# Kernel tuning notes

Hardware: AMD Instinct MI355X
Metric: run time of the kernel (lower is better)

The kernel has to match this reference:

```python
import jax, jax.numpy as jnp
import numpy as np
import math

B, S, HID, NH = 2, 2048, 1024, 16
HD = HID // NH  # head_dim = 64
TEMPERATURE = 1.0


def setup_inputs() -> dict:
    key = jax.random.key(0)
    ks = jax.random.split(key, 6)
    w = lambda k: (jax.random.normal(k, (HID, HID), dtype=jnp.float32) * 0.02)
    return {
        "hidden_states": jax.random.normal(ks[0], (B, S, HID), dtype=jnp.float32),
        "attention_mask": jnp.ones((B, S), dtype=jnp.float32),
        "Wq": w(ks[1]), "bq": jnp.zeros((HID,), jnp.float32),
        "Wk": w(ks[2]), "bk": jnp.zeros((HID,), jnp.float32),
        "Wv": w(ks[3]), "bv": jnp.zeros((HID,), jnp.float32),
        "Wo": w(ks[4]), "bo": jnp.zeros((HID,), jnp.float32),
    }


def reference(hidden_states, attention_mask, Wq, bq, Wk, bk, Wv, bv, Wo, bo):
    b, s, hid = hidden_states.shape
    heads = lambda x: x.reshape(b, s, NH, HD).transpose(0, 2, 1, 3)  # [b,h,s,d]

    q = heads(hidden_states @ Wq.T + bq)
    k = heads(hidden_states @ Wk.T + bk)
    v = heads(hidden_states @ Wv.T + bv)

    # padding mask applied multiplicatively to k and v
    m = attention_mask[:, None, :, None]  # [b,1,s,1]
    k = k * m
    v = v * m

    # auxiliary Hopfield state: k^T @ v per head -> [b,h,d,d]
    state = jnp.einsum("bhsd,bhse->bhde", k, v)

    # energy / scores
    energy = jnp.einsum("bhqd,bhkd->bhqk", q, k) / (TEMPERATURE * math.sqrt(HD))
    causal = jnp.triu(jnp.ones((s, s), dtype=bool), k=1)  # True above diagonal
    energy = jnp.where(causal[None, None], -jnp.inf, energy)
    energy = jnp.where(attention_mask[:, None, None, :] == 0, -jnp.inf, energy)

    attn = jax.nn.softmax(energy, axis=-1)
    out = jnp.einsum("bhqk,bhkd->bhqd", attn, v)
    out = out.transpose(0, 2, 1, 3).reshape(b, s, hid)
    out = out @ Wo.T + bo
    return out, state
```

## Files before the change

### kernel.cpp

```cpp
#include <hip/hip_runtime.h>
#include <hip/hip_bf16.h>

#define B_ 2
#define S_ 2048
#define HID_ 1024
#define NH_ 16
#define HD_ 64
#define MTOK (B_*S_)
#define LDQKV 3072

typedef __attribute__((ext_vector_type(8))) __bf16 bf16x8;
typedef __attribute__((ext_vector_type(4))) __bf16 bf16x4;
typedef __attribute__((ext_vector_type(4))) float f32x4;

__device__ __forceinline__ void gl16(__bf16* lds, const __bf16* g) {
  __builtin_amdgcn_global_load_lds(
      (const __attribute__((address_space(1))) void*)g,
      (__attribute__((address_space(3))) void*)lds, 16, 0, 0);
}
__device__ __forceinline__ void gl4(float* lds, const float* g) {
  __builtin_amdgcn_global_load_lds(
      (const __attribute__((address_space(1))) void*)g,
      (__attribute__((address_space(3))) void*)lds, 4, 0, 0);
}

__global__ __launch_bounds__(256) void cast_all(
    const float* __restrict__ X,
    const float* __restrict__ Wq, const float* __restrict__ Wk,
    const float* __restrict__ Wv, const float* __restrict__ Wo,
    __bf16* __restrict__ Xb, __bf16* __restrict__ Wqkvb, __bf16* __restrict__ Wob)
{
  int i = blockIdx.x * 256 + threadIdx.x;
  const float* src; __bf16* dst; int j;
  if (i < (1 << 20))              { src = X;  dst = Xb;                 j = i; }
  else if (i < (1<<20)+(1<<18))   { src = Wq; dst = Wqkvb;              j = i - (1<<20); }
  else if (i < (1<<20)+(2<<18))   { src = Wk; dst = Wqkvb + (1<<20);    j = i - (1<<20) - (1<<18); }
  else if (i < (1<<20)+(3<<18))   { src = Wv; dst = Wqkvb + (2<<20);    j = i - (1<<20) - (2<<18); }
  else                            { src = Wo; dst = Wob;                j = i - (1<<20) - (3<<18); }
  float4 v = reinterpret_cast<const float4*>(src)[j];
  bf16x4 o;
  o[0] = (__bf16)v.x; o[1] = (__bf16)v.y; o[2] = (__bf16)v.z; o[3] = (__bf16)v.w;
  reinterpret_cast<bf16x4*>(dst)[j] = o;
}

__global__ __launch_bounds__(256) void gemm_qkv(
    const __bf16* __restrict__ A, const __bf16* __restrict__ W,
    const float* __restrict__ bq, const float* __restrict__ bk,
    const float* __restrict__ bv, const float* __restrict__ mask,
    __bf16* __restrict__ C)
{
  __shared__ __bf16 As[128 * 32];
  __shared__ __bf16 Bs[128 * 32];
  const int t = threadIdx.x;
  const int m0 = blockIdx.y * 128;
  const int n0 = blockIdx.x * 128;
  const int lane = t & 63;
  const int w = t >> 6;
  const int wr = (w >> 1) * 64;
  const int wc = (w & 1) * 64;
  const int fr = lane & 15;
  const int kg = lane >> 4;

  f32x4 acc[4][4];
  #pragma unroll
  for (int i = 0; i < 4; i++)
    #pragma unroll
    for (int j = 0; j < 4; j++) acc[i][j] = (f32x4)0.f;

  const int srow = w * 16 + (lane >> 2);
  const int scol = (lane & 3) * 8;
  const __bf16* ap0 = A + (size_t)(m0 + srow) * HID_ + scol;
  const __bf16* ap1 = A + (size_t)(m0 + 64 + srow) * HID_ + scol;
  const __bf16* wp0 = W + (size_t)(n0 + srow) * HID_ + scol;
  const __bf16* wp1 = W + (size_t)(n0 + 64 + srow) * HID_ + scol;

  for (int k0 = 0; k0 < HID_; k0 += 32) {
    __syncthreads();
    gl16(&As[w * 512], ap0 + k0);
    gl16(&As[2048 + w * 512], ap1 + k0);
    gl16(&Bs[w * 512], wp0 + k0);
    gl16(&Bs[2048 + w * 512], wp1 + k0);
    __syncthreads();
    bf16x8 af[4], bf[4];
    #pragma unroll
    for (int m = 0; m < 4; m++) af[m] = *(const bf16x8*)&As[(wr + m*16 + fr) * 32 + kg*8];
    #pragma unroll
    for (int n = 0; n < 4; n++) bf[n] = *(const bf16x8*)&Bs[(wc + n*16 + fr) * 32 + kg*8];
    #pragma unroll
    for (int m = 0; m < 4; m++)
      #pragma unroll
      for (int n = 0; n < 4; n++)
        acc[m][n] = __builtin_amdgcn_mfma_f32_16x16x32_bf16(af[m], bf[n], acc[m][n], 0, 0, 0);
  }

  const int region = n0 >> 10;
  const float* bias = region == 0 ? bq : (region == 1 ? bk : bv);
  const int nloc = n0 & 1023;

  #pragma unroll
  for (int m = 0; m < 4; m++) {
    #pragma unroll
    for (int r = 0; r < 4; r++) {
      int row = m0 + wr + m*16 + kg*4 + r;
      float rs = region ? mask[row] : 1.f;
      #pragma unroll
      for (int n = 0; n < 4; n++) {
        int c = wc + n*16 + fr;
        float v = (acc[m][n][r] + bias[nloc + c]) * rs;
        C[(size_t)row * LDQKV + n0 + c] = (__bf16)v;
      }
    }
  }
}

__global__ __launch_bounds__(256) void gemm_o(
    const __bf16* __restrict__ A, const __bf16* __restrict__ W,
    const float* __restrict__ bias, float* __restrict__ C)
{
  __shared__ __bf16 As[128 * 32];
  __shared__ __bf16 Bs[128 * 32];
  const int t = threadIdx.x;
  const int m0 = blockIdx.y * 128;
  const int n0 = blockIdx.x * 128;
  const int lane = t & 63;
  const int w = t >> 6;
  const int wr = (w >> 1) * 64;
  const int wc = (w & 1) * 64;
  const int fr = lane & 15;
  const int kg = lane >> 4;

  f32x4 acc[4][4];
  #pragma unroll
  for (int i = 0; i < 4; i++)
    #pragma unroll
    for (int j = 0; j < 4; j++) acc[i][j] = (f32x4)0.f;

  const int srow = w * 16 + (lane >> 2);
  const int scol = (lane & 3) * 8;
  const __bf16* ap0 = A + (size_t)(m0 + srow) * HID_ + scol;
  const __bf16* ap1 = A + (size_t)(m0 + 64 + srow) * HID_ + scol;
  const __bf16* wp0 = W + (size_t)(n0 + srow) * HID_ + scol;
  const __bf16* wp1 = W + (size_t)(n0 + 64 + srow) * HID_ + scol;

  for (int k0 = 0; k0 < HID_; k0 += 32) {
    __syncthreads();
    gl16(&As[w * 512], ap0 + k0);
    gl16(&As[2048 + w * 512], ap1 + k0);
    gl16(&Bs[w * 512], wp0 + k0);
    gl16(&Bs[2048 + w * 512], wp1 + k0);
    __syncthreads();
    bf16x8 af[4], bf[4];
    #pragma unroll
    for (int m = 0; m < 4; m++) af[m] = *(const bf16x8*)&As[(wr + m*16 + fr) * 32 + kg*8];
    #pragma unroll
    for (int n = 0; n < 4; n++) bf[n] = *(const bf16x8*)&Bs[(wc + n*16 + fr) * 32 + kg*8];
    #pragma unroll
    for (int m = 0; m < 4; m++)
      #pragma unroll
      for (int n = 0; n < 4; n++)
        acc[m][n] = __builtin_amdgcn_mfma_f32_16x16x32_bf16(af[m], bf[n], acc[m][n], 0, 0, 0);
  }

  #pragma unroll
  for (int m = 0; m < 4; m++) {
    #pragma unroll
    for (int r = 0; r < 4; r++) {
      int row = m0 + wr + m*16 + kg*4 + r;
      #pragma unroll
      for (int n = 0; n < 4; n++) {
        int col = n0 + wc + n*16 + fr;
        C[(size_t)row * HID_ + col] = acc[m][n][r] + bias[col];
      }
    }
  }
}

__global__ __launch_bounds__(256) void transpose_bf16(
    const __bf16* __restrict__ in, int ldin, __bf16* __restrict__ out)
{
  __shared__ __bf16 tile[64][68];
  const int tok0 = blockIdx.x * 64;
  const int f0 = blockIdx.y * 64;
  const int t = threadIdx.x;
  const int r = t >> 2;
  const int c0 = (t & 3) * 16;
  const __bf16* src = in + (size_t)(tok0 + r) * ldin + f0 + c0;
  *(bf16x8*)&tile[r][c0]     = *(const bf16x8*)src;
  *(bf16x8*)&tile[r][c0 + 8] = *(const bf16x8*)(src + 8);
  __syncthreads();
  bf16x8 o0, o1;
  #pragma unroll
  for (int j = 0; j < 8; j++) { o0[j] = tile[c0 + j][r]; o1[j] = tile[c0 + 8 + j][r]; }
  __bf16* dst = out + (size_t)(f0 + r) * MTOK + tok0 + c0;
  *(bf16x8*)dst = o0;
  *(bf16x8*)(dst + 8) = o1;
}

#define SCALE_LOG2E 0.18033688011112043f

__device__ __forceinline__ bf16x8 ld_swz(const __bf16* base, int row, int xb) {
  return *(const bf16x8*)((const char*)base + row * 128 + (xb ^ ((row & 7) << 4)));
}
__device__ __forceinline__ void st_swz16(__bf16* base, int row, int colbyte, __bf16 v) {
  *(__bf16*)((char*)base + row * 128 + (colbyte ^ ((row & 7) << 4))) = v;
}
__device__ __forceinline__ bf16x8 ld_swz256(const __bf16* base, int row, int xb) {
  return *(const bf16x8*)((const char*)base + row * 256 + (xb ^ ((row & 7) << 4)));
}

__global__ __launch_bounds__(512) void flash_mfma(
    const __bf16* __restrict__ Q, const __bf16* __restrict__ K,
    const __bf16* __restrict__ Vt, const float* __restrict__ mask,
    __bf16* __restrict__ O)
{
  __shared__ __bf16 Ks[2][64 * 64];
  __shared__ __bf16 Vs[2][64 * 64];
  __shared__ __bf16 Ps[8][16 * 64];
  __shared__ float mk[2][64];

  const int bh = blockIdx.x;
  const int qt = (int)(gridDim.y - 1) - (int)blockIdx.y;
  const int b = bh >> 4, h = bh & 15;
  const int t = threadIdx.x;
  const int w = t >> 6;
  const int lane = t & 63;
  const int fc = lane & 15;
  const int kg = lane >> 4;
  const int g4 = kg * 4;

  const int q0w = qt * 128 + w * 16;
  const size_t tokbase = (size_t)b * S_;

  const int rr = lane >> 3;
  const int cswz = ((lane & 7) ^ rr) * 8;
  const int ktmax = 2 * qt + 1;

  gl16(&Ks[0][w * 512], K + (tokbase + (size_t)(w * 8 + rr)) * LDQKV + h * HD_ + cswz);
  gl16(&Vs[0][w * 512], Vt + (size_t)(h * HD_ + w * 8 + rr) * MTOK + tokbase + cswz);
  gl4(&mk[0][0], mask + tokbase + lane);

  bf16x8 qa[2];
  {
    const __bf16* qp = Q + (tokbase + q0w + fc) * LDQKV + h * HD_;
    qa[0] = *(const bf16x8*)(qp + kg * 8);
    qa[1] = *(const bf16x8*)(qp + 32 + kg * 8);
  }

  bf16x8 ones;
  #pragma unroll
  for (int j = 0; j < 8; j++) ones[j] = (__bf16)1.f;

  f32x4 acc[4], accl;
  #pragma unroll
  for (int n = 0; n < 4; n++) acc[n] = (f32x4)0.f;
  accl = (f32x4)0.f;

  __bf16* pw = &Ps[w][0];

  for (int kt = 0; kt <= ktmax; ++kt) {
    const int cur = kt & 1;
    if (kt < ktmax) {
      const int nxt = cur ^ 1;
      gl16(&Ks[nxt][w * 512],
           K + (tokbase + (size_t)((kt + 1) * 64 + w * 8 + rr)) * LDQKV + h * HD_ + cswz);
      gl16(&Vs[nxt][w * 512],
           Vt + (size_t)(h * HD_ + w * 8 + rr) * MTOK + tokbase + (kt + 1) * 64 + cswz);
      gl4(&mk[nxt][0], mask + tokbase + (kt + 1) * 64 + lane);
      asm volatile("s_waitcnt vmcnt(3)" ::: "memory");
    } else {
      asm volatile("s_waitcnt vmcnt(0)" ::: "memory");
    }
    __builtin_amdgcn_sched_barrier(0);
    __builtin_amdgcn_s_barrier();

    if (kt * 64 <= q0w + 15) {
      const __bf16* ks = &Ks[cur][0];
      const __bf16* vs = &Vs[cur][0];
      f32x4 s[4];
      #pragma unroll
      for (int n = 0; n < 4; n++) s[n] = (f32x4)0.f;
      #pragma unroll
      for (int kd = 0; kd < 2; kd++)
        #pragma unroll
        for (int n = 0; n < 4; n++) {
          bf16x8 kf = ld_swz(ks, n * 16 + fc, kd * 64 + kg * 16);
          s[n] = __builtin_amdgcn_mfma_f32_16x16x32_bf16(qa[kd], kf, s[n], 0, 0, 0);
        }

      bool okm[4];
      #pragma unroll
      for (int n = 0; n < 4; n++) okm[n] = (mk[cur][n * 16 + fc] != 0.f);

      const bool fullt = (kt * 64 + 63 <= q0w);
      if (fullt) {
        #pragma unroll
        for (int r = 0; r < 4; r++)
          #pragma unroll
          for (int n = 0; n < 4; n++) {
            float p = okm[n] ? exp2f(s[n][r] * SCALE_LOG2E) : 0.f;
            st_swz16(pw, g4 + r, (n * 16 + fc) * 2, (__bf16)p);
          }
      } else {
        #pragma unroll
        for (int r = 0; r < 4; r++) {
          const int qg = q0w + g4 + r;
          #pragma unroll
          for (int n = 0; n < 4; n++) {
            bool ok = okm[n] && (kt * 64 + n * 16 + fc <= qg);
            float p = ok ? exp2f(s[n][r] * SCALE_LOG2E) : 0.f;
            st_swz16(pw, g4 + r, (n * 16 + fc) * 2, (__bf16)p);
          }
        }
      }

      #pragma unroll
      for (int kc = 0; kc < 2; kc++) {
        bf16x8 pf = ld_swz(pw, fc, kc * 64 + kg * 16);
        accl = __builtin_amdgcn_mfma_f32_16x16x32_bf16(pf, ones, accl, 0, 0, 0);
        #pragma unroll
        for (int n = 0; n < 4; n++) {
          bf16x8 vf = ld_swz(vs, n * 16 + fc, kc * 64 + kg * 16);
          acc[n] = __builtin_amdgcn_mfma_f32_16x16x32_bf16(pf, vf, acc[n], 0, 0, 0);
        }
      }
    }
    __builtin_amdgcn_s_barrier();
  }

  #pragma unroll
  for (int r = 0; r < 4; r++) {
    float inv = accl[r] > 0.f ? 1.f / accl[r] : 0.f;
    __bf16* op = O + (tokbase + q0w + g4 + r) * HID_ + h * HD_;
    #pragma unroll
    for (int n = 0; n < 4; n++)
      op[n * 16 + fc] = (__bf16)(acc[n][r] * inv);
  }
}

__global__ __launch_bounds__(256) void state_mfma(
    const __bf16* __restrict__ Kt, const __bf16* __restrict__ Vt,
    float* __restrict__ part)
{
  __shared__ __bf16 Kl[64 * 128];
  __shared__ __bf16 Vl[64 * 128];
  const int bh = blockIdx.x, sc = blockIdx.y;
  const int b = bh >> 4, h = bh & 15;
  const int t = threadIdx.x;
  const int w = t >> 6;
  const int lane = t & 63;
  const int fc = lane & 15;
  const int kg = lane >> 4;
  const size_t colbase = (size_t)b * S_ + sc * 128;
  const int rloc = lane >> 4;
  const int cb = (lane & 15) * 16;

  #pragma unroll
  for (int c = 0; c < 4; c++) {
    int row = w * 16 + c * 4 + rloc;
    int scol = (cb ^ ((row & 7) << 4)) >> 1;
    gl16(&Kl[(w * 16 + c * 4) * 128], Kt + (size_t)(h * HD_ + row) * MTOK + colbase + scol);
    gl16(&Vl[(w * 16 + c * 4) * 128], Vt + (size_t)(h * HD_ + row) * MTOK + colbase + scol);
  }
  __syncthreads();

  f32x4 acc[4];
  #pragma unroll
  for (int n = 0; n < 4; n++) acc[n] = (f32x4)0.f;
  #pragma unroll
  for (int ks = 0; ks < 4; ks++) {
    bf16x8 af = ld_swz256(Kl, w * 16 + fc, ks * 64 + kg * 16);
    #pragma unroll
    for (int n = 0; n < 4; n++) {
      bf16x8 bfr = ld_swz256(Vl, n * 16 + fc, ks * 64 + kg * 16);
      acc[n] = __builtin_amdgcn_mfma_f32_16x16x32_bf16(af, bfr, acc[n], 0, 0, 0);
    }
  }

  float* dst = part + (((size_t)bh * 16 + sc) << 12);
  #pragma unroll
  for (int n = 0; n < 4; n++)
    #pragma unroll
    for (int r = 0; r < 4; r++)
      dst[(w * 16 + kg * 4 + r) * 64 + n * 16 + fc] = acc[n][r];
}

__global__ __launch_bounds__(256) void state_reduce(
    const float* __restrict__ part, float* __restrict__ out)
{
  int i = blockIdx.x * 256 + threadIdx.x;
  int bh = i >> 12, de = i & 4095;
  float s = 0.f;
  #pragma unroll
  for (int sc = 0; sc < 16; sc++) s += part[(((size_t)bh * 16 + sc) << 12) + de];
  out[i] = s;
}

extern "C" void kernel_launch(void* const* d_in, const int* in_sizes, int n_in,
                              void* d_out, int out_size, void* d_ws, size_t ws_size,
                              hipStream_t stream)
{
  const float* hs   = (const float*)d_in[0];
  const float* mask = (const float*)d_in[1];
  const float* Wq   = (const float*)d_in[2];
  const float* bq   = (const float*)d_in[3];
  const float* Wk   = (const float*)d_in[4];
  const float* bk   = (const float*)d_in[5];
  const float* Wv   = (const float*)d_in[6];
  const float* bv   = (const float*)d_in[7];
  const float* Wo   = (const float*)d_in[8];
  const float* bo   = (const float*)d_in[9];
  float* out = (float*)d_out;

  char* ws = (char*)d_ws;
  __bf16* Wqkvb = (__bf16*)(ws);
  __bf16* Wob   = (__bf16*)(ws + (6u  << 20));
  __bf16* Xb    = (__bf16*)(ws + (8u  << 20));
  __bf16* QKV   = (__bf16*)(ws + (16u << 20));
  __bf16* Ob    = (__bf16*)(ws + (40u << 20));
  float*  part  = (float*)(ws + (48u << 20));

  cast_all<<<8192, 256, 0, stream>>>(hs, Wq, Wk, Wv, Wo, Xb, Wqkvb, Wob);

  gemm_qkv<<<dim3(LDQKV / 128, MTOK / 128), 256, 0, stream>>>(
      Xb, Wqkvb, bq, bk, bv, mask, QKV);

  __bf16* Vtg = Xb;
  transpose_bf16<<<dim3(MTOK / 64, HID_ / 64), 256, 0, stream>>>(QKV + 2048, LDQKV, Vtg);

  flash_mfma<<<dim3(B_ * NH_, S_ / 128), 512, 0, stream>>>(
      QKV, QKV + 1024, Vtg, mask, Ob);

  gemm_o<<<dim3(HID_ / 128, MTOK / 128), 256, 0, stream>>>(Ob, Wob, bo, out);

  __bf16* Ktg = Wqkvb;
  transpose_bf16<<<dim3(MTOK / 64, HID_ / 64), 256, 0, stream>>>(QKV + 1024, LDQKV, Ktg);

  state_mfma<<<dim3(B_ * NH_, 16), 256, 0, stream>>>(Ktg, Vtg, part);
  state_reduce<<<512, 256, 0, stream>>>(part, out + (size_t)MTOK * HID_);
}
```

Before: 144.1 us.

## Double-buffer GEMM loads, shrink flash tiles to 64 queries, merge K/V transposes

```diff
diff --git a/kernel.cpp b/kernel.cpp
--- a/kernel.cpp
+++ b/kernel.cpp
@@ -49,8 +49,8 @@
     const float* __restrict__ bv, const float* __restrict__ mask,
     __bf16* __restrict__ C)
 {
-  __shared__ __bf16 As[128 * 32];
-  __shared__ __bf16 Bs[128 * 32];
+  __shared__ __bf16 As[2][128 * 32];
+  __shared__ __bf16 Bs[2][128 * 32];
   const int t = threadIdx.x;
   const int m0 = blockIdx.y * 128;
   const int n0 = blockIdx.x * 128;
@@ -74,23 +74,34 @@
   const __bf16* wp0 = W + (size_t)(n0 + srow) * HID_ + scol;
   const __bf16* wp1 = W + (size_t)(n0 + 64 + srow) * HID_ + scol;
 
+  #define GSTAGE(buf, koff) \
+    gl16(&As[buf][w * 512], ap0 + (koff)); \
+    gl16(&As[buf][2048 + w * 512], ap1 + (koff)); \
+    gl16(&Bs[buf][w * 512], wp0 + (koff)); \
+    gl16(&Bs[buf][2048 + w * 512], wp1 + (koff));
+
+  GSTAGE(0, 0);
   for (int k0 = 0; k0 < HID_; k0 += 32) {
-    __syncthreads();
-    gl16(&As[w * 512], ap0 + k0);
-    gl16(&As[2048 + w * 512], ap1 + k0);
-    gl16(&Bs[w * 512], wp0 + k0);
-    gl16(&Bs[2048 + w * 512], wp1 + k0);
-    __syncthreads();
+    const int cur = (k0 >> 5) & 1;
+    if (k0 + 32 < HID_) {
+      GSTAGE(cur ^ 1, k0 + 32);
+      asm volatile("s_waitcnt vmcnt(4)" ::: "memory");
+    } else {
+      asm volatile("s_waitcnt vmcnt(0)" ::: "memory");
+    }
+    __builtin_amdgcn_sched_barrier(0);
+    __builtin_amdgcn_s_barrier();
     bf16x8 af[4], bf[4];
     #pragma unroll
-    for (int m = 0; m < 4; m++) af[m] = *(const bf16x8*)&As[(wr + m*16 + fr) * 32 + kg*8];
-    #pragma unroll
-    for (int n = 0; n < 4; n++) bf[n] = *(const bf16x8*)&Bs[(wc + n*16 + fr) * 32 + kg*8];
+    for (int m = 0; m < 4; m++) af[m] = *(const bf16x8*)&As[cur][(wr + m*16 + fr) * 32 + kg*8];
+    #pragma unroll
+    for (int n = 0; n < 4; n++) bf[n] = *(const bf16x8*)&Bs[cur][(wc + n*16 + fr) * 32 + kg*8];
     #pragma unroll
     for (int m = 0; m < 4; m++)
       #pragma unroll
       for (int n = 0; n < 4; n++)
         acc[m][n] = __builtin_amdgcn_mfma_f32_16x16x32_bf16(af[m], bf[n], acc[m][n], 0, 0, 0);
+    __builtin_amdgcn_s_barrier();
   }
 
   const int region = n0 >> 10;
@@ -117,8 +128,8 @@
     const __bf16* __restrict__ A, const __bf16* __restrict__ W,
     const float* __restrict__ bias, float* __restrict__ C)
 {
-  __shared__ __bf16 As[128 * 32];
-  __shared__ __bf16 Bs[128 * 32];
+  __shared__ __bf16 As[2][128 * 32];
+  __shared__ __bf16 Bs[2][128 * 32];
   const int t = threadIdx.x;
   const int m0 = blockIdx.y * 128;
   const int n0 = blockIdx.x * 128;
@@ -142,23 +153,28 @@
   const __bf16* wp0 = W + (size_t)(n0 + srow) * HID_ + scol;
   const __bf16* wp1 = W + (size_t)(n0 + 64 + srow) * HID_ + scol;
 
+  GSTAGE(0, 0);
   for (int k0 = 0; k0 < HID_; k0 += 32) {
-    __syncthreads();
-    gl16(&As[w * 512], ap0 + k0);
-    gl16(&As[2048 + w * 512], ap1 + k0);
-    gl16(&Bs[w * 512], wp0 + k0);
-    gl16(&Bs[2048 + w * 512], wp1 + k0);
-    __syncthreads();
+    const int cur = (k0 >> 5) & 1;
+    if (k0 + 32 < HID_) {
+      GSTAGE(cur ^ 1, k0 + 32);
+      asm volatile("s_waitcnt vmcnt(4)" ::: "memory");
+    } else {
+      asm volatile("s_waitcnt vmcnt(0)" ::: "memory");
+    }
+    __builtin_amdgcn_sched_barrier(0);
+    __builtin_amdgcn_s_barrier();
     bf16x8 af[4], bf[4];
     #pragma unroll
-    for (int m = 0; m < 4; m++) af[m] = *(const bf16x8*)&As[(wr + m*16 + fr) * 32 + kg*8];
-    #pragma unroll
-    for (int n = 0; n < 4; n++) bf[n] = *(const bf16x8*)&Bs[(wc + n*16 + fr) * 32 + kg*8];
+    for (int m = 0; m < 4; m++) af[m] = *(const bf16x8*)&As[cur][(wr + m*16 + fr) * 32 + kg*8];
+    #pragma unroll
+    for (int n = 0; n < 4; n++) bf[n] = *(const bf16x8*)&Bs[cur][(wc + n*16 + fr) * 32 + kg*8];
     #pragma unroll
     for (int m = 0; m < 4; m++)
       #pragma unroll
       for (int n = 0; n < 4; n++)
         acc[m][n] = __builtin_amdgcn_mfma_f32_16x16x32_bf16(af[m], bf[n], acc[m][n], 0, 0, 0);
+    __builtin_amdgcn_s_barrier();
   }
 
   #pragma unroll
@@ -175,16 +191,19 @@
   }
 }
 
-__global__ __launch_bounds__(256) void transpose_bf16(
-    const __bf16* __restrict__ in, int ldin, __bf16* __restrict__ out)
+__global__ __launch_bounds__(256) void transpose_kv(
+    const __bf16* __restrict__ Kin, const __bf16* __restrict__ Vin,
+    __bf16* __restrict__ Kt, __bf16* __restrict__ Vt)
 {
   __shared__ __bf16 tile[64][68];
   const int tok0 = blockIdx.x * 64;
   const int f0 = blockIdx.y * 64;
+  const __bf16* in = blockIdx.z ? Vin : Kin;
+  __bf16* out = blockIdx.z ? Vt : Kt;
   const int t = threadIdx.x;
   const int r = t >> 2;
   const int c0 = (t & 3) * 16;
-  const __bf16* src = in + (size_t)(tok0 + r) * ldin + f0 + c0;
+  const __bf16* src = in + (size_t)(tok0 + r) * LDQKV + f0 + c0;
   *(bf16x8*)&tile[r][c0]     = *(const bf16x8*)src;
   *(bf16x8*)&tile[r][c0 + 8] = *(const bf16x8*)(src + 8);
   __syncthreads();
@@ -208,18 +227,70 @@
   return *(const bf16x8*)((const char*)base + row * 256 + (xb ^ ((row & 7) << 4)));
 }
 
-__global__ __launch_bounds__(512) void flash_mfma(
+__device__ __forceinline__ void attn_tile(
+    const __bf16* __restrict__ ks, const __bf16* __restrict__ vs,
+    const bool (&okm)[4], __bf16* __restrict__ pw,
+    const bf16x8 (&qa)[2], f32x4 (&acc)[4], f32x4& accl,
+    const bf16x8 ones, int q0w, int kt, int fc, int kg)
+{
+  f32x4 s[4];
+  #pragma unroll
+  for (int n = 0; n < 4; n++) s[n] = (f32x4)0.f;
+  #pragma unroll
+  for (int kd = 0; kd < 2; kd++)
+    #pragma unroll
+    for (int n = 0; n < 4; n++) {
+      bf16x8 kf = ld_swz(ks, n * 16 + fc, kd * 64 + kg * 16);
+      s[n] = __builtin_amdgcn_mfma_f32_16x16x32_bf16(qa[kd], kf, s[n], 0, 0, 0);
+    }
+
+  const int g4 = kg * 4;
+  const bool fullt = (kt * 64 + 63 <= q0w);
+  if (fullt) {
+    #pragma unroll
+    for (int r = 0; r < 4; r++)
+      #pragma unroll
+      for (int n = 0; n < 4; n++) {
+        float p = okm[n] ? exp2f(s[n][r] * SCALE_LOG2E) : 0.f;
+        st_swz16(pw, g4 + r, (n * 16 + fc) * 2, (__bf16)p);
+      }
+  } else {
+    #pragma unroll
+    for (int r = 0; r < 4; r++) {
+      const int qg = q0w + g4 + r;
+      #pragma unroll
+      for (int n = 0; n < 4; n++) {
+        bool ok = okm[n] && (kt * 64 + n * 16 + fc <= qg);
+        float p = ok ? exp2f(s[n][r] * SCALE_LOG2E) : 0.f;
+        st_swz16(pw, g4 + r, (n * 16 + fc) * 2, (__bf16)p);
+      }
+    }
+  }
+
+  #pragma unroll
+  for (int kc = 0; kc < 2; kc++) {
+    bf16x8 pf = ld_swz(pw, fc, kc * 64 + kg * 16);
+    accl = __builtin_amdgcn_mfma_f32_16x16x32_bf16(pf, ones, accl, 0, 0, 0);
+    #pragma unroll
+    for (int n = 0; n < 4; n++) {
+      bf16x8 vf = ld_swz(vs, n * 16 + fc, kc * 64 + kg * 16);
+      acc[n] = __builtin_amdgcn_mfma_f32_16x16x32_bf16(pf, vf, acc[n], 0, 0, 0);
+    }
+  }
+}
+
+__global__ __launch_bounds__(256) void flash_mfma(
     const __bf16* __restrict__ Q, const __bf16* __restrict__ K,
     const __bf16* __restrict__ Vt, const float* __restrict__ mask,
     __bf16* __restrict__ O)
 {
   __shared__ __bf16 Ks[2][64 * 64];
   __shared__ __bf16 Vs[2][64 * 64];
-  __shared__ __bf16 Ps[8][16 * 64];
+  __shared__ __bf16 Ps[4][16 * 64];
   __shared__ float mk[2][64];
 
   const int bh = blockIdx.x;
-  const int qt = (int)(gridDim.y - 1) - (int)blockIdx.y;
+  const int qt = 31 - (int)blockIdx.y;
   const int b = bh >> 4, h = bh & 15;
   const int t = threadIdx.x;
   const int w = t >> 6;
@@ -228,15 +299,17 @@
   const int kg = lane >> 4;
   const int g4 = kg * 4;
 
-  const int q0w = qt * 128 + w * 16;
+  const int q0w = qt * 64 + w * 16;
   const size_t tokbase = (size_t)b * S_;
 
   const int rr = lane >> 3;
   const int cswz = ((lane & 7) ^ rr) * 8;
-  const int ktmax = 2 * qt + 1;
-
-  gl16(&Ks[0][w * 512], K + (tokbase + (size_t)(w * 8 + rr)) * LDQKV + h * HD_ + cswz);
-  gl16(&Vs[0][w * 512], Vt + (size_t)(h * HD_ + w * 8 + rr) * MTOK + tokbase + cswz);
+  const int ktmax = qt;
+
+  gl16(&Ks[0][(w * 16) * 64],     K + (tokbase + (size_t)(w * 16 + rr)) * LDQKV + h * HD_ + cswz);
+  gl16(&Ks[0][(w * 16 + 8) * 64], K + (tokbase + (size_t)(w * 16 + 8 + rr)) * LDQKV + h * HD_ + cswz);
+  gl16(&Vs[0][(w * 16) * 64],     Vt + (size_t)(h * HD_ + w * 16 + rr) * MTOK + tokbase + cswz);
+  gl16(&Vs[0][(w * 16 + 8) * 64], Vt + (size_t)(h * HD_ + w * 16 + 8 + rr) * MTOK + tokbase + cswz);
   gl4(&mk[0][0], mask + tokbase + lane);
 
   bf16x8 qa[2];
@@ -261,69 +334,25 @@
     const int cur = kt & 1;
     if (kt < ktmax) {
       const int nxt = cur ^ 1;
-      gl16(&Ks[nxt][w * 512],
-           K + (tokbase + (size_t)((kt + 1) * 64 + w * 8 + rr)) * LDQKV + h * HD_ + cswz);
-      gl16(&Vs[nxt][w * 512],
-           Vt + (size_t)(h * HD_ + w * 8 + rr) * MTOK + tokbase + (kt + 1) * 64 + cswz);
+      const size_t krow = tokbase + (size_t)((kt + 1) * 64);
+      gl16(&Ks[nxt][(w * 16) * 64],     K + (krow + w * 16 + rr) * LDQKV + h * HD_ + cswz);
+      gl16(&Ks[nxt][(w * 16 + 8) * 64], K + (krow + w * 16 + 8 + rr) * LDQKV + h * HD_ + cswz);
+      gl16(&Vs[nxt][(w * 16) * 64],     Vt + (size_t)(h * HD_ + w * 16 + rr) * MTOK + tokbase + (kt + 1) * 64 + cswz);
+      gl16(&Vs[nxt][(w * 16 + 8) * 64], Vt + (size_t)(h * HD_ + w * 16 + 8 + rr) * MTOK + tokbase + (kt + 1) * 64 + cswz);
       gl4(&mk[nxt][0], mask + tokbase + (kt + 1) * 64 + lane);
-      asm volatile("s_waitcnt vmcnt(3)" ::: "memory");
+      asm volatile("s_waitcnt vmcnt(5)" ::: "memory");
     } else {
       asm volatile("s_waitcnt vmcnt(0)" ::: "memory");
     }
     __builtin_amdgcn_sched_barrier(0);
     __builtin_amdgcn_s_barrier();
 
-    if (kt * 64 <= q0w + 15) {
-      const __bf16* ks = &Ks[cur][0];
-      const __bf16* vs = &Vs[cur][0];
-      f32x4 s[4];
-      #pragma unroll
-      for (int n = 0; n < 4; n++) s[n] = (f32x4)0.f;
-      #pragma unroll
-      for (int kd = 0; kd < 2; kd++)
-        #pragma unroll
-        for (int n = 0; n < 4; n++) {
-          bf16x8 kf = ld_swz(ks, n * 16 + fc, kd * 64 + kg * 16);
-          s[n] = __builtin_amdgcn_mfma_f32_16x16x32_bf16(qa[kd], kf, s[n], 0, 0, 0);
-        }
-
-      bool okm[4];
-      #pragma unroll
-      for (int n = 0; n < 4; n++) okm[n] = (mk[cur][n * 16 + fc] != 0.f);
-
-      const bool fullt = (kt * 64 + 63 <= q0w);
-      if (fullt) {
-        #pragma unroll
-        for (int r = 0; r < 4; r++)
-          #pragma unroll
-          for (int n = 0; n < 4; n++) {
-            float p = okm[n] ? exp2f(s[n][r] * SCALE_LOG2E) : 0.f;
-            st_swz16(pw, g4 + r, (n * 16 + fc) * 2, (__bf16)p);
-          }
-      } else {
-        #pragma unroll
-        for (int r = 0; r < 4; r++) {
-          const int qg = q0w + g4 + r;
-          #pragma unroll
-          for (int n = 0; n < 4; n++) {
-            bool ok = okm[n] && (kt * 64 + n * 16 + fc <= qg);
-            float p = ok ? exp2f(s[n][r] * SCALE_LOG2E) : 0.f;
-            st_swz16(pw, g4 + r, (n * 16 + fc) * 2, (__bf16)p);
-          }
-        }
-      }
-
-      #pragma unroll
-      for (int kc = 0; kc < 2; kc++) {
-        bf16x8 pf = ld_swz(pw, fc, kc * 64 + kg * 16);
-        accl = __builtin_amdgcn_mfma_f32_16x16x32_bf16(pf, ones, accl, 0, 0, 0);
-        #pragma unroll
-        for (int n = 0; n < 4; n++) {
-          bf16x8 vf = ld_swz(vs, n * 16 + fc, kc * 64 + kg * 16);
-          acc[n] = __builtin_amdgcn_mfma_f32_16x16x32_bf16(pf, vf, acc[n], 0, 0, 0);
-        }
-      }
-    }
+    bool okm[4];
+    #pragma unroll
+    for (int n = 0; n < 4; n++) okm[n] = (mk[cur][n * 16 + fc] != 0.f);
+
+    attn_tile(&Ks[cur][0], &Vs[cur][0], okm, pw, qa, acc, accl, ones, q0w, kt, fc, kg);
+
     __builtin_amdgcn_s_barrier();
   }
 
@@ -417,7 +446,7 @@
   __bf16* Xb    = (__bf16*)(ws + (8u  << 20));
   __bf16* QKV   = (__bf16*)(ws + (16u << 20));
   __bf16* Ob    = (__bf16*)(ws + (40u << 20));
-  float*  part  = (float*)(ws + (48u << 20));
+  __bf16* Ktg   = (__bf16*)(ws + (48u << 20));
 
   cast_all<<<8192, 256, 0, stream>>>(hs, Wq, Wk, Wv, Wo, Xb, Wqkvb, Wob);
 
@@ -425,16 +454,15 @@
       Xb, Wqkvb, bq, bk, bv, mask, QKV);
 
   __bf16* Vtg = Xb;
-  transpose_bf16<<<dim3(MTOK / 64, HID_ / 64), 256, 0, stream>>>(QKV + 2048, LDQKV, Vtg);
-
-  flash_mfma<<<dim3(B_ * NH_, S_ / 128), 512, 0, stream>>>(
+  transpose_kv<<<dim3(MTOK / 64, HID_ / 64, 2), 256, 0, stream>>>(
+      QKV + 1024, QKV + 2048, Ktg, Vtg);
+
+  flash_mfma<<<dim3(B_ * NH_, 32), 256, 0, stream>>>(
       QKV, QKV + 1024, Vtg, mask, Ob);
 
   gemm_o<<<dim3(HID_ / 128, MTOK / 128), 256, 0, stream>>>(Ob, Wob, bo, out);
 
-  __bf16* Ktg = Wqkvb;
-  transpose_bf16<<<dim3(MTOK / 64, HID_ / 64), 256, 0, stream>>>(QKV + 1024, LDQKV, Ktg);
-
+  float* part = (float*)Ob;
   state_mfma<<<dim3(B_ * NH_, 16), 256, 0, stream>>>(Ktg, Vtg, part);
   state_reduce<<<512, 256, 0, stream>>>(part, out + (size_t)MTOK * HID_);
 }
```

After: 140.9 us. -2.2%, faster.
